# Performance work log

Hardware: AMD Instinct MI355X
Metric: run time of the kernel (lower is better)

## Reference

```python
import jax, jax.numpy as jnp
import numpy as np

ALPHA = 0.5  # distance-decay base (self.alpha)

def setup_inputs() -> dict:
    key = jax.random.key(0)
    N, E, D_IN, D_OUT = 50000, 800000, 128, 128
    k1, k2, k3, k4, k5 = jax.random.split(key, 5)
    h = jax.random.normal(k1, (N, D_IN), dtype=jnp.float32)
    # first N edges are self-loops so every node has in/out degree >= 1
    src = jnp.concatenate([jnp.arange(N), jax.random.randint(k2, (E - N,), 0, N)]).astype(jnp.int32)
    dst = jnp.concatenate([jnp.arange(N), jax.random.randint(k3, (E - N,), 0, N)]).astype(jnp.int32)
    distance = jax.random.randint(k4, (E,), 0, 6).astype(jnp.int32)
    limit = float(np.sqrt(6.0 / (D_IN + D_OUT)))  # xavier_uniform
    weight = jax.random.uniform(k5, (D_IN, D_OUT), jnp.float32, -limit, limit)
    bias = jnp.zeros((D_OUT,), jnp.float32)
    return {"h": h, "src": src, "dst": dst, "distance": distance, "weight": weight, "bias": bias}

def reference(h, src, dst, distance, weight, bias):
    N = h.shape[0]
    ones = jnp.ones(src.shape[0], jnp.float32)
    out_deg = jax.ops.segment_sum(ones, src, num_segments=N)  # [N]
    in_deg = jax.ops.segment_sum(ones, dst, num_segments=N)   # [N]
    # source-side symmetric norm
    feat = h * (out_deg ** -0.5)[:, None]                     # [N, D]
    # per-edge message: gathered src feature * alpha^distance
    w = jnp.power(jnp.float32(ALPHA), distance.astype(jnp.float32))  # [E]
    msg = feat[src] * w[:, None]                              # [E, D]
    # mean over mailbox == segment-sum / in-degree
    agg = jax.ops.segment_sum(msg, dst, num_segments=N) / in_deg[:, None]  # [N, D]
    rst = agg @ weight                                        # [N, D_OUT]
    rst = rst * (in_deg ** -0.5)[:, None] + bias
    return rst
```

## Files before the change

### kernel.cpp

```cpp
#include <hip/hip_runtime.h>


constexpr int D = 128;
constexpr int HC = 32;
constexpr int PNODES = 32;
constexpr int PCAP = 768;
constexpr int CHUNK = 8192;
constexpr int NCAST = 384;

typedef __attribute__((ext_vector_type(8))) short bf16x8;
typedef __attribute__((ext_vector_type(4))) float f32x4;
typedef __attribute__((ext_vector_type(2))) _Float16 f16x2;

__device__ __forceinline__ float bf16_to_f(unsigned int u16) {
    union { unsigned int u; float f; } c; c.u = u16 << 16; return c.f;
}
__device__ __forceinline__ unsigned int f_to_bf16(float f) {
    union { float f; unsigned int u; } c; c.f = f;
    unsigned int u = c.u;
    u += 0x7fffu + ((u >> 16) & 1u);
    return u >> 16;
}
__device__ __forceinline__ unsigned int pack_f16x2(float x, float y) {
    f16x2 p; p.x = (_Float16)x; p.y = (_Float16)y;
    union { f16x2 h; unsigned int u; } c; c.h = p; return c.u;
}

__global__ __launch_bounds__(256) void k_combo(const int* __restrict__ src,
        const int* __restrict__ dst, const int* __restrict__ dist,
        int* __restrict__ gcur, unsigned int* __restrict__ gbuf,
        unsigned int* __restrict__ gdeg,
        const float4* __restrict__ h4, uint4* __restrict__ hs4,
        const float* __restrict__ W, unsigned short* __restrict__ Wt,
        int E, int N, int NW, int hchunk, int P, int nbA) {
    extern __shared__ int dyn[];
    int tid = threadIdx.x;
    int bi = blockIdx.x;

    if (bi >= nbA + HC) {
        if (bi == nbA + HC) {
            for (int i = tid; i < D * D; i += 256) {
                int k = i >> 7, n = i & 127;
                Wt[n * D + k] = (unsigned short)f_to_bf16(W[i]);
            }
            return;
        }
        int cb = bi - (nbA + HC + 1);
        int G = N * (D / 8);
        for (int i = cb * 256 + tid; i < G; i += NCAST * 256) {
            float4 a = h4[2 * i];
            float4 b = h4[2 * i + 1];
            uint4 o;
            o.x = pack_f16x2(a.x, a.y);
            o.y = pack_f16x2(a.z, a.w);
            o.z = pack_f16x2(b.x, b.y);
            o.w = pack_f16x2(b.z, b.w);
            hs4[i] = o;
        }
        return;
    }

    if (bi >= nbA) {
        unsigned int* bins = (unsigned int*)dyn;
        for (int i = tid; i < NW; i += 256) bins[i] = 0;
        __syncthreads();
        int c = bi - nbA;
        int e0 = c * hchunk, e1 = min(e0 + hchunk, E);
        for (int i = e0 + tid * 4; i < e1; i += 1024) {
            if (i + 3 < e1) {
                int4 k4 = *(const int4*)&src[i];
                atomicAdd(&bins[k4.x >> 1], 1u << ((k4.x & 1) * 16));
                atomicAdd(&bins[k4.y >> 1], 1u << ((k4.y & 1) * 16));
                atomicAdd(&bins[k4.z >> 1], 1u << ((k4.z & 1) * 16));
                atomicAdd(&bins[k4.w >> 1], 1u << ((k4.w & 1) * 16));
            } else {
                for (int e = i; e < e1; e++)
                    atomicAdd(&bins[src[e] >> 1], 1u << ((src[e] & 1) * 16));
            }
        }
        __syncthreads();
        for (int i = tid; i < NW; i += 256) {
            unsigned int v = bins[i];
            if (v) atomicAdd(&gdeg[i], v);
        }
        return;
    }

    unsigned int* sorted = (unsigned int*)dyn;
    int* gidx  = dyn + CHUNK;
    int* hist  = dyn + 2 * CHUNK;
    int* start = hist + P;
    int* lofs  = start + P;
    int* base_g = lofs + P;
    __shared__ int wsum[4];

    int lane = tid & 63, w = tid >> 6;
    int e0 = bi * CHUNK;
    int e1 = min(e0 + CHUNK, E);
    int ce = e1 - e0;

    for (int b = tid; b < P; b += 256) hist[b] = 0;
    __syncthreads();

    for (int i = e0 + tid * 4; i < e1; i += 1024) {
        if (i + 3 < e1) {
            int4 d4 = *(const int4*)&dst[i];
            atomicAdd(&hist[d4.x >> 5], 1);
            atomicAdd(&hist[d4.y >> 5], 1);
            atomicAdd(&hist[d4.z >> 5], 1);
            atomicAdd(&hist[d4.w >> 5], 1);
        } else {
            for (int e = i; e < e1; e++) atomicAdd(&hist[dst[e] >> 5], 1);
        }
    }
    __syncthreads();

    int loc[7];
    int s = 0;
    #pragma unroll
    for (int j = 0; j < 7; j++) {
        int b = tid * 7 + j;
        int v = (b < P) ? hist[b] : 0;
        loc[j] = s;
        s += v;
    }
    int x = s;
    #pragma unroll
    for (int off = 1; off < 64; off <<= 1) {
        int t = __shfl_up(x, off, 64);
        if (lane >= off) x += t;
    }
    if (lane == 63) wsum[w] = x;
    __syncthreads();
    int tbase = x - s;
    #pragma unroll
    for (int k = 0; k < 4; k++) if (k < w) tbase += wsum[k];
    #pragma unroll
    for (int j = 0; j < 7; j++) {
        int b = tid * 7 + j;
        if (b < P) {
            int st = tbase + loc[j];
            start[b] = st;
            lofs[b] = st;
            int cnt = hist[b];
            if (cnt) base_g[b] = atomicAdd(&gcur[b], cnt);
        }
    }
    __syncthreads();

    for (int i = e0 + tid * 4; i < e1; i += 1024) {
        if (i + 3 < e1) {
            int4 s4 = *(const int4*)&src[i];
            int4 d4 = *(const int4*)&dst[i];
            int4 q4 = *(const int4*)&dist[i];
            #pragma unroll
            for (int j = 0; j < 4; j++) {
                int sv = (&s4.x)[j], dv = (&d4.x)[j], qv = (&q4.x)[j];
                int p = dv >> 5;
                unsigned int wd = (unsigned)sv | ((unsigned)(dv & 31) << 16)
                                | ((unsigned)qv << 21);
                int pos = atomicAdd(&lofs[p], 1);
                sorted[pos] = wd;
                int rank = base_g[p] + (pos - start[p]);
                gidx[pos] = (rank < PCAP) ? p * PCAP + rank : -1;
            }
        } else {
            for (int e = i; e < e1; e++) {
                int sv = src[e], dv = dst[e], qv = dist[e];
                int p = dv >> 5;
                unsigned int wd = (unsigned)sv | ((unsigned)(dv & 31) << 16)
                                | ((unsigned)qv << 21);
                int pos = atomicAdd(&lofs[p], 1);
                sorted[pos] = wd;
                int rank = base_g[p] + (pos - start[p]);
                gidx[pos] = (rank < PCAP) ? p * PCAP + rank : -1;
            }
        }
    }
    __syncthreads();

    for (int i = tid; i < ce; i += 256) {
        int g = gidx[i];
        if (g >= 0) gbuf[g] = sorted[i];
    }
}

__global__ __launch_bounds__(256, 6) void k_pagg(const uint4* __restrict__ hs4,
        const unsigned int* __restrict__ gbuf, const int* __restrict__ gcur,
        const unsigned short* __restrict__ gdeg16,
        const unsigned short* __restrict__ Wt, const float* __restrict__ bias,
        float* __restrict__ out, int N) {
    __shared__ unsigned int elist[PCAP];
    __shared__ unsigned int slist[PCAP];
    __shared__ int h2[PNODES], st2[PNODES], lo2[PNODES];
    __shared__ unsigned short As[PNODES * 136];
    int p = blockIdx.x;
    int tid = threadIdx.x;
    int cnt = min(gcur[p], PCAP);
    const unsigned int* gp = gbuf + (size_t)p * PCAP;

    if (tid < PNODES) h2[tid] = 0;
    __syncthreads();
    for (int i = tid; i < cnt; i += 256) {
        unsigned int wd = gp[i];
        elist[i] = wd;
        atomicAdd(&h2[(wd >> 16) & 31], 1);
    }
    __syncthreads();
    if (tid < 64) {
        int v = (tid < PNODES) ? h2[tid] : 0;
        int x = v;
        #pragma unroll
        for (int off = 1; off < 32; off <<= 1) {
            int t = __shfl_up(x, off, 64);
            if ((tid & 63) >= off) x += t;
        }
        if (tid < PNODES) { st2[tid] = x - v; lo2[tid] = x - v; }
    }
    __syncthreads();
    for (int i = tid; i < cnt; i += 256) {
        unsigned int wd = elist[i];
        int pos = atomicAdd(&lo2[(wd >> 16) & 31], 1);
        slist[pos] = wd;
    }
    __syncthreads();

    int wv = tid >> 6, l64 = tid & 63;
    int lane16 = l64 & 15, sub = l64 >> 4;
    #pragma unroll
    for (int k = 0; k < 8; k++) {
        int dl = wv * 8 + k;
        int node = p * PNODES + dl;
        int deg = h2[dl], b = st2[dl];
        float acc[8] = {0.f, 0.f, 0.f, 0.f, 0.f, 0.f, 0.f, 0.f};
        for (int eo = 0; eo < deg; eo += 32) {
            uint4 hv[8];
            float cc[8];
            #pragma unroll
            for (int j = 0; j < 8; j++) {
                if (eo + j * 4 < deg) {
                    int off = eo + j * 4 + sub;
                    bool valid = off < deg;
                    unsigned int wd = slist[b + (valid ? off : 0)];
                    unsigned int sv = wd & 0xffffu;
                    float os = rsqrtf((float)gdeg16[sv]);
                    cc[j] = valid
                        ? __uint_as_float((127u - ((wd >> 21) & 7u)) << 23) * os
                        : 0.f;
                    hv[j] = hs4[(sv << 4) + (unsigned)lane16];
                }
            }
            #pragma unroll
            for (int j = 0; j < 8; j++) {
                if (eo + j * 4 < deg) {
                    float c = cc[j];
                    const f16x2* hp = (const f16x2*)&hv[j];
                    #pragma unroll
                    for (int q = 0; q < 4; q++) {
                        acc[2 * q]     = fmaf((float)hp[q].x, c, acc[2 * q]);
                        acc[2 * q + 1] = fmaf((float)hp[q].y, c, acc[2 * q + 1]);
                    }
                }
            }
        }
        #pragma unroll
        for (int j = 0; j < 8; j++) {
            acc[j] += __shfl_xor(acc[j], 16, 64);
            acc[j] += __shfl_xor(acc[j], 32, 64);
        }
        if (sub == 0) {
            uint4 o = make_uint4(0u, 0u, 0u, 0u);
            if (node < N) {
                float fd = (float)deg;
                float sc = rsqrtf(fd) / fd;
                o.x = f_to_bf16(acc[0] * sc) | (f_to_bf16(acc[1] * sc) << 16);
                o.y = f_to_bf16(acc[2] * sc) | (f_to_bf16(acc[3] * sc) << 16);
                o.z = f_to_bf16(acc[4] * sc) | (f_to_bf16(acc[5] * sc) << 16);
                o.w = f_to_bf16(acc[6] * sc) | (f_to_bf16(acc[7] * sc) << 16);
            }
            *(uint4*)&As[dl * 136 + lane16 * 8] = o;
        }
    }
    __syncthreads();

    int m = l64 & 15, quad = l64 >> 4;
    int mt = wv & 1, ntb = (wv >> 1) * 4;
    f32x4 acc2[4];
    #pragma unroll
    for (int t = 0; t < 4; t++) acc2[t] = (f32x4){0.f, 0.f, 0.f, 0.f};
    #pragma unroll
    for (int s = 0; s < 4; s++) {
        bf16x8 a = *(const bf16x8*)&As[(mt * 16 + m) * 136 + quad * 8 + s * 32];
        #pragma unroll
        for (int t = 0; t < 4; t++) {
            int n = (ntb + t) * 16 + m;
            bf16x8 b = *(const bf16x8*)&Wt[n * D + quad * 8 + s * 32];
            acc2[t] = __builtin_amdgcn_mfma_f32_16x16x32_bf16(a, b, acc2[t], 0, 0, 0);
        }
    }
    int orow0 = p * PNODES + mt * 16 + quad * 4;
    #pragma unroll
    for (int t = 0; t < 4; t++) {
        int n = (ntb + t) * 16 + m;
        float bz = bias[n];
        #pragma unroll
        for (int r = 0; r < 4; r++) {
            int grow = orow0 + r;
            if (grow < N) out[(size_t)grow * D + n] = acc2[t][r] + bz;
        }
    }
}

extern "C" void kernel_launch(void* const* d_in, const int* in_sizes, int n_in,
                              void* d_out, int out_size, void* d_ws, size_t ws_size,
                              hipStream_t stream) {
    const float* h    = (const float*)d_in[0];
    const int*   src  = (const int*)d_in[1];
    const int*   dst  = (const int*)d_in[2];
    const int*   dist = (const int*)d_in[3];
    const float* W    = (const float*)d_in[4];
    const float* bias = (const float*)d_in[5];
    float* out = (float*)d_out;
    const int N = in_sizes[0] / D;
    const int E = in_sizes[1];

    const int NW = (N + 1) / 2;
    const int hchunk = (((E + HC - 1) / HC) + 3) & ~3;
    const int P = (N + PNODES - 1) / PNODES;
    const int nbA = (E + CHUNK - 1) / CHUNK;

    char* ws = (char*)d_ws;
    size_t p = 0;
    auto alloc = [&](size_t bytes) -> char* {
        char* r = ws + p;
        p = (p + bytes + 511) & ~(size_t)511;
        return r;
    };
    int* gcur = (int*)alloc((size_t)P * 4);
    unsigned int* gdeg = (unsigned int*)alloc((size_t)NW * 4);
    unsigned int* gbuf = (unsigned int*)alloc((size_t)P * PCAP * 4);
    unsigned short* hs = (unsigned short*)alloc((size_t)N * D * 2);
    unsigned short* Wt = (unsigned short*)alloc((size_t)D * D * 2);

    size_t dyn_part = ((size_t)2 * CHUNK + 4 * P) * 4;
    size_t dyn_hist = (size_t)NW * 4;
    size_t dyn_sz = dyn_part > dyn_hist ? dyn_part : dyn_hist;

    hipMemsetAsync(gcur, 0, (size_t)((char*)gdeg - (char*)gcur) + (size_t)NW * 4,
                   stream);
    k_combo<<<nbA + HC + 1 + NCAST, 256, dyn_sz, stream>>>(src, dst, dist,
            gcur, gbuf, gdeg, (const float4*)h, (uint4*)hs, W, Wt,
            E, N, NW, hchunk, P, nbA);
    k_pagg<<<P, 256, 0, stream>>>((const uint4*)hs, gbuf, gcur,
            (const unsigned short*)gdeg, Wt, bias, out, N);
}
```

Baseline: 156.3 us.

## Assign one node per 16-lane group, pack degree bins, halve partition chunk

The aggregation phase now gives each 16-lane group its own destination node and walks that node's edges 8 at a time. The old scheme spread each node across the whole wave and then reduced with cross-lane shuffles, which wasted lanes on low-degree nodes. The out-degree histogram now packs four 8-bit counters per LDS word instead of two 16-bit ones, halving shared memory per block, then unpacks them into 16-bit global counters. The edge partition chunk is halved to launch more partition blocks. The 8-bit per-block counters risk overflow if one source appears more than 255 times in a histogram chunk, and padded iterations load a duplicate edge with a zero weight.

```diff
diff --git a/kernel.cpp b/kernel.cpp
--- a/kernel.cpp
+++ b/kernel.cpp
@@ -5,7 +5,7 @@
 constexpr int HC = 32;
 constexpr int PNODES = 32;
 constexpr int PCAP = 768;
-constexpr int CHUNK = 8192;
+constexpr int CHUNK = 4096;
 constexpr int NCAST = 384;
 
 typedef __attribute__((ext_vector_type(8))) short bf16x8;
@@ -32,7 +32,7 @@
         unsigned int* __restrict__ gdeg,
         const float4* __restrict__ h4, uint4* __restrict__ hs4,
         const float* __restrict__ W, unsigned short* __restrict__ Wt,
-        int E, int N, int NW, int hchunk, int P, int nbA) {
+        int E, int N, int NW, int NB, int hchunk, int P, int nbA) {
     extern __shared__ int dyn[];
     int tid = threadIdx.x;
     int bi = blockIdx.x;
@@ -62,26 +62,31 @@
 
     if (bi >= nbA) {
         unsigned int* bins = (unsigned int*)dyn;
-        for (int i = tid; i < NW; i += 256) bins[i] = 0;
+        for (int i = tid; i < NB; i += 256) bins[i] = 0;
         __syncthreads();
         int c = bi - nbA;
         int e0 = c * hchunk, e1 = min(e0 + hchunk, E);
         for (int i = e0 + tid * 4; i < e1; i += 1024) {
             if (i + 3 < e1) {
                 int4 k4 = *(const int4*)&src[i];
-                atomicAdd(&bins[k4.x >> 1], 1u << ((k4.x & 1) * 16));
-                atomicAdd(&bins[k4.y >> 1], 1u << ((k4.y & 1) * 16));
-                atomicAdd(&bins[k4.z >> 1], 1u << ((k4.z & 1) * 16));
-                atomicAdd(&bins[k4.w >> 1], 1u << ((k4.w & 1) * 16));
+                atomicAdd(&bins[k4.x >> 2], 1u << ((k4.x & 3) * 8));
+                atomicAdd(&bins[k4.y >> 2], 1u << ((k4.y & 3) * 8));
+                atomicAdd(&bins[k4.z >> 2], 1u << ((k4.z & 3) * 8));
+                atomicAdd(&bins[k4.w >> 2], 1u << ((k4.w & 3) * 8));
             } else {
                 for (int e = i; e < e1; e++)
-                    atomicAdd(&bins[src[e] >> 1], 1u << ((src[e] & 1) * 16));
+                    atomicAdd(&bins[src[e] >> 2], 1u << ((src[e] & 3) * 8));
             }
         }
         __syncthreads();
-        for (int i = tid; i < NW; i += 256) {
+        for (int i = tid; i < NB; i += 256) {
             unsigned int v = bins[i];
-            if (v) atomicAdd(&gdeg[i], v);
+            if (v) {
+                unsigned int lo = (v & 0xffu) | ((v & 0xff00u) << 8);
+                unsigned int hi = ((v >> 16) & 0xffu) | ((v >> 8) & 0xff0000u);
+                if (lo) atomicAdd(&gdeg[2 * i], lo);
+                if (hi && 2 * i + 1 < NW) atomicAdd(&gdeg[2 * i + 1], hi);
+            }
         }
         return;
     }
@@ -226,60 +231,49 @@
     __syncthreads();
 
     int wv = tid >> 6, l64 = tid & 63;
-    int lane16 = l64 & 15, sub = l64 >> 4;
-    #pragma unroll
-    for (int k = 0; k < 8; k++) {
-        int dl = wv * 8 + k;
-        int node = p * PNODES + dl;
+    int grp = l64 >> 4;
+    int lane16 = l64 & 15;
+    #pragma unroll
+    for (int half = 0; half < 2; half++) {
+        int dl = half * 16 + wv * 4 + grp;
         int deg = h2[dl], b = st2[dl];
         float acc[8] = {0.f, 0.f, 0.f, 0.f, 0.f, 0.f, 0.f, 0.f};
-        for (int eo = 0; eo < deg; eo += 32) {
+        for (int eo = 0; eo < deg; eo += 8) {
             uint4 hv[8];
             float cc[8];
             #pragma unroll
             for (int j = 0; j < 8; j++) {
-                if (eo + j * 4 < deg) {
-                    int off = eo + j * 4 + sub;
-                    bool valid = off < deg;
-                    unsigned int wd = slist[b + (valid ? off : 0)];
-                    unsigned int sv = wd & 0xffffu;
-                    float os = rsqrtf((float)gdeg16[sv]);
-                    cc[j] = valid
-                        ? __uint_as_float((127u - ((wd >> 21) & 7u)) << 23) * os
-                        : 0.f;
-                    hv[j] = hs4[(sv << 4) + (unsigned)lane16];
-                }
+                int off = eo + j;
+                int ei = b + (off < deg ? off : deg - 1);
+                unsigned int wd = slist[ei];
+                unsigned int sv = wd & 0xffffu;
+                float os = rsqrtf((float)gdeg16[sv]);
+                cc[j] = (off < deg)
+                    ? __uint_as_float((127u - ((wd >> 21) & 7u)) << 23) * os
+                    : 0.f;
+                hv[j] = hs4[(sv << 4) + (unsigned)lane16];
             }
             #pragma unroll
             for (int j = 0; j < 8; j++) {
-                if (eo + j * 4 < deg) {
-                    float c = cc[j];
-                    const f16x2* hp = (const f16x2*)&hv[j];
-                    #pragma unroll
-                    for (int q = 0; q < 4; q++) {
-                        acc[2 * q]     = fmaf((float)hp[q].x, c, acc[2 * q]);
-                        acc[2 * q + 1] = fmaf((float)hp[q].y, c, acc[2 * q + 1]);
-                    }
+                float c = cc[j];
+                const f16x2* hp = (const f16x2*)&hv[j];
+                #pragma unroll
+                for (int q = 0; q < 4; q++) {
+                    acc[2 * q]     = fmaf((float)hp[q].x, c, acc[2 * q]);
+                    acc[2 * q + 1] = fmaf((float)hp[q].y, c, acc[2 * q + 1]);
                 }
             }
         }
-        #pragma unroll
-        for (int j = 0; j < 8; j++) {
-            acc[j] += __shfl_xor(acc[j], 16, 64);
-            acc[j] += __shfl_xor(acc[j], 32, 64);
-        }
-        if (sub == 0) {
-            uint4 o = make_uint4(0u, 0u, 0u, 0u);
-            if (node < N) {
-                float fd = (float)deg;
-                float sc = rsqrtf(fd) / fd;
-                o.x = f_to_bf16(acc[0] * sc) | (f_to_bf16(acc[1] * sc) << 16);
-                o.y = f_to_bf16(acc[2] * sc) | (f_to_bf16(acc[3] * sc) << 16);
-                o.z = f_to_bf16(acc[4] * sc) | (f_to_bf16(acc[5] * sc) << 16);
-                o.w = f_to_bf16(acc[6] * sc) | (f_to_bf16(acc[7] * sc) << 16);
-            }
-            *(uint4*)&As[dl * 136 + lane16 * 8] = o;
-        }
+        uint4 o = make_uint4(0u, 0u, 0u, 0u);
+        if (p * PNODES + dl < N && deg > 0) {
+            float fd = (float)deg;
+            float sc = rsqrtf(fd) / fd;
+            o.x = f_to_bf16(acc[0] * sc) | (f_to_bf16(acc[1] * sc) << 16);
+            o.y = f_to_bf16(acc[2] * sc) | (f_to_bf16(acc[3] * sc) << 16);
+            o.z = f_to_bf16(acc[4] * sc) | (f_to_bf16(acc[5] * sc) << 16);
+            o.w = f_to_bf16(acc[6] * sc) | (f_to_bf16(acc[7] * sc) << 16);
+        }
+        *(uint4*)&As[dl * 136 + lane16 * 8] = o;
     }
     __syncthreads();
 
@@ -325,6 +319,7 @@
     const int E = in_sizes[1];
 
     const int NW = (N + 1) / 2;
+    const int NB = (N + 3) / 4;
     const int hchunk = (((E + HC - 1) / HC) + 3) & ~3;
     const int P = (N + PNODES - 1) / PNODES;
     const int nbA = (E + CHUNK - 1) / CHUNK;
@@ -343,14 +338,14 @@
     unsigned short* Wt = (unsigned short*)alloc((size_t)D * D * 2);
 
     size_t dyn_part = ((size_t)2 * CHUNK + 4 * P) * 4;
-    size_t dyn_hist = (size_t)NW * 4;
+    size_t dyn_hist = (size_t)NB * 4;
     size_t dyn_sz = dyn_part > dyn_hist ? dyn_part : dyn_hist;
 
     hipMemsetAsync(gcur, 0, (size_t)((char*)gdeg - (char*)gcur) + (size_t)NW * 4,
                    stream);
     k_combo<<<nbA + HC + 1 + NCAST, 256, dyn_sz, stream>>>(src, dst, dist,
             gcur, gbuf, gdeg, (const float4*)h, (uint4*)hs, W, Wt,
-            E, N, NW, hchunk, P, nbA);
+            E, N, NW, NB, hchunk, P, nbA);
     k_pagg<<<P, 256, 0, stream>>>((const uint4*)hs, gbuf, gcur,
             (const unsigned short*)gdeg, Wt, bias, out, N);
 }
```

Result: slower. 209.7 us (+34.2%).
